# Kernel optimization log

Hardware: AMD Instinct MI355X
Metric: run time of the kernel (lower is better)

Reference implementation:

```python
import jax, jax.numpy as jnp
import numpy as np

B, T, L = 64, 512, 48
START, PAD, END = 46, 45, 47


def setup_inputs() -> dict:
    key = jax.random.key(0)
    k1, k2, k3 = jax.random.split(key, 3)
    scores = jax.random.normal(k1, (B, T, L), dtype=jnp.float32)
    gold_target = jax.random.randint(k2, (B, T), 0, L, dtype=jnp.int64)
    trans = jax.random.normal(k3, (L, L), dtype=jnp.float32)
    # replicate the in-place constraint initialization from __init__ (order matters)
    trans = trans.at[:, START].set(-10000.0)
    trans = trans.at[END, :].set(-10000.0)
    trans = trans.at[PAD, :].set(-10000.0)
    trans = trans.at[PAD, END].set(0.0)
    trans = trans.at[PAD, PAD].set(0.0)
    trans = trans.at[START, :].set(0.0)
    mask = jnp.ones((B, T), dtype=jnp.int32)
    return {"scores": scores, "gold_target": gold_target, "mask": mask, "transitions": trans}


def reference(scores, gold_target, mask, transitions):
    Bn, Tn, Ln = scores.shape
    # crf_scores[t, b, from, to] = emission(b, t, from) + transitions[from, to]  (time-major)
    crf = scores.transpose(1, 0, 2)[:, :, :, None] + transitions[None, None]      # (T, B, L, L)
    start = jnp.broadcast_to(transitions[None, None], (1, Bn, Ln, Ln))
    crf = jnp.concatenate([start, crf], axis=0)                                   # (T+1, B, L, L)

    # gold energy: faithful to original torch.gather on flattened (L*L) with raw tag index
    gold = jnp.concatenate(
        [jnp.full((1, Bn), START, dtype=gold_target.dtype), gold_target.T], axis=0)  # (T+1, B)
    flat = crf.reshape(Tn + 1, Bn, Ln * Ln)
    tg = jnp.take_along_axis(flat, gold[:, :, None], axis=2)[:, :, 0]             # (T+1, B)
    maskp = jnp.concatenate([jnp.ones((1, Bn), mask.dtype), mask.T], axis=0)      # (T+1, B)
    tg_energy = jnp.sum(tg * maskp.astype(tg.dtype))

    # forward algorithm (stable log-sum-exp recurrence) via lax.scan
    init = crf[0, :, START, :]                                                    # (B, L)
    def step(fs, xs):
        trans_t, m_t = xs                                                         # (B,L,L), (B,)
        nxt = jax.nn.logsumexp(fs[:, :, None] + trans_t, axis=1)                  # (B, L)
        fs = jnp.where(m_t[:, None].astype(bool), nxt, fs)
        return fs, None
    fs, _ = jax.lax.scan(step, init, (crf[1:], maskp[1:]))
    forscore = fs[:, END].sum()

    return (forscore - tg_energy) / Bn
```

## Files before the change

kernel.cpp:

```cpp
#include <hip/hip_runtime.h>

#define Bn 64
#define Tn 512
#define Ln 48
#define START_L 46
#define PAD_L 45
#define END_L 47
#define QP 72
#define LSEG 8
#define NBUF 16
#define NCHUNK (Tn / (LSEG * NBUF))

typedef __bf16 bf16x8 __attribute__((ext_vector_type(8)));
typedef float f32x4 __attribute__((ext_vector_type(4)));
#define MFMA __builtin_amdgcn_mfma_f32_16x16x32_bf16

__device__ __forceinline__ unsigned short f2bf(float x) {
    unsigned u = __float_as_uint(x);
    u += 0x7fffu + ((u >> 16) & 1u);
    return (unsigned short)(u >> 16);
}
__device__ __forceinline__ unsigned pkT(float a, float b) {
    return __builtin_amdgcn_perm(__float_as_uint(b), __float_as_uint(a), 0x07060302u);
}
__device__ __forceinline__ float bcast0(float x) {
    return __int_as_float(__builtin_amdgcn_readfirstlane(__float_as_int(x)));
}
__device__ __forceinline__ float4 exp4(float4 v) {
    float4 r; r.x = __expf(v.x); r.y = __expf(v.y); r.z = __expf(v.z); r.w = __expf(v.w);
    return r;
}


__device__ __forceinline__ void readTB(const unsigned short* buf, int c, int q, bf16x8 F[3][2]) {
    #pragma unroll
    for (int x = 0; x < 3; ++x) {
        F[x][0] = *(const bf16x8*)&buf[(x * 16 + c) * QP + q * 8];
        F[x][1] = *(const bf16x8*)&buf[(x * 16 + c) * QP + 32 + q * 8];
    }
}

__device__ __forceinline__ void storeTB(unsigned short* buf, int c, int q,
                                        const f32x4 (&acc)[3][3],
                                        float4 w0, float4 w1, float4 w2) {
    #pragma unroll
    for (int nt = 0; nt < 3; ++nt) {
        unsigned u0 = pkT(acc[0][nt][0] * w0.x, acc[0][nt][1] * w0.y);
        unsigned u1 = pkT(acc[0][nt][2] * w0.z, acc[0][nt][3] * w0.w);
        unsigned u2 = pkT(acc[1][nt][0] * w1.x, acc[1][nt][1] * w1.y);
        unsigned u3 = pkT(acc[1][nt][2] * w1.z, acc[1][nt][3] * w1.w);
        unsigned u4 = pkT(acc[2][nt][0] * w2.x, acc[2][nt][1] * w2.y);
        unsigned u5 = pkT(acc[2][nt][2] * w2.z, acc[2][nt][3] * w2.w);
        unsigned short* wp = &buf[(nt * 16 + c) * QP + q * 16];
        uint4 s4; s4.x = u0; s4.y = u1; s4.z = u2; s4.w = u3;
        *(uint4*)wp = s4;
        uint2 s2; s2.x = u4; s2.y = u5;
        *(uint2*)(wp + 8) = s2;
    }
}

__device__ __forceinline__ float treeProd(const unsigned short* bufA, const unsigned short* bufB,
                                          unsigned short* dst, int c, int q) {
    bf16x8 FA[3][2], FB[3][2];
    readTB(bufA, c, q, FA);
    readTB(bufB, c, q, FB);
    f32x4 acc[3][3];
    const f32x4 z = {0.f, 0.f, 0.f, 0.f};
    #pragma unroll
    for (int mt = 0; mt < 3; ++mt)
        #pragma unroll
        for (int nt = 0; nt < 3; ++nt) {
            acc[mt][nt] = MFMA(FA[mt][0], FB[nt][0], z, 0, 0, 0);
            acc[mt][nt] = MFMA(FA[mt][1], FB[nt][1], acc[mt][nt], 0, 0, 0);
        }
    float r = bcast0(acc[0][0][0]);
    float rr = __builtin_amdgcn_rcpf(r);
    float4 w; w.x = rr; w.y = rr; w.z = rr; w.w = rr;
    storeTB(dst, c, q, acc, w, w, w);
    return __logf(r);
}

__global__ __launch_bounds__(512, 2) void scan_k(
        const float* __restrict__ scores,
        const float* __restrict__ trans,
        unsigned short* __restrict__ ws2M,
        float* __restrict__ ws2S,
        float* __restrict__ out) {
    const int b   = blockIdx.x & (Bn - 1);
    const int cid = blockIdx.x >> 6;
    const int tid = threadIdx.x;
    const int w   = tid >> 6;
    const int lane = tid & 63;
    const int c = lane & 15;
    const int q = lane >> 4;

    __shared__ __align__(16) unsigned short TBs[NBUF][48 * QP];
    __shared__ float scl[32];

    for (int i = tid; i < NBUF * 48 * QP / 4; i += 512)
        ((unsigned long long*)TBs)[i] = 0ull;
    __syncthreads();

    const int dirOdd = w & 1;
    const int s1 = cid * NBUF + w;
    const int s2 = s1 + 8;
    const int t0a = s1 * LSEG, tea = t0a + LSEG - 1;
    const int t0b = s2 * LSEG, teb = t0b + LSEG - 1;
    const float* sb = scores + (size_t)b * Tn * Ln;

    bf16x8 A[3][2];
    #pragma unroll
    for (int mt = 0; mt < 3; ++mt)
        #pragma unroll
        for (int kt = 0; kt < 2; ++kt) {
            union { unsigned u[4]; bf16x8 v; } fu;
            #pragma unroll
            for (int j2 = 0; j2 < 4; ++j2) {
                int kk0 = kt * 32 + q * 8 + 2 * j2;
                int rem = kk0 & 15;
                if (rem < 12) {
                    int row0 = (rem >> 2) * 16 + (kk0 >> 4) * 4 + (kk0 & 3);
                    float tv0 = dirOdd ? trans[(mt * 16 + c) * Ln + row0]
                                       : trans[row0 * Ln + mt * 16 + c];
                    float tv1 = dirOdd ? trans[(mt * 16 + c) * Ln + row0 + 1]
                                       : trans[(row0 + 1) * Ln + mt * 16 + c];
                    fu.u[j2] = pkT(__expf(tv0), __expf(tv1));
                } else fu.u[j2] = 0u;
            }
            A[mt][kt] = fu.v;
        }

    unsigned short* TB0 = TBs[w];
    unsigned short* TB1 = TBs[w + 8];

    if (lane < Ln) {
        int m16 = lane >> 4, q4 = (lane >> 2) & 3, r = lane & 3;
        int kk = q4 * 16 + m16 * 4 + r;
        TB0[lane * QP + kk] = dirOdd ? (unsigned short)0x3F80
                                     : f2bf(__expf(sb[(size_t)t0a * Ln + lane]));
        TB1[lane * QP + kk] = dirOdd ? (unsigned short)0x3F80
                                     : f2bf(__expf(sb[(size_t)t0b * Ln + lane]));
    }

    auto clampA = [&](int t) { return t < t0a ? t0a : (t > tea ? tea : t); };
    auto clampB = [&](int t) { return t < t0b ? t0b : (t > teb ? teb : t); };

    float4 wA0, wA1, wA2, wB0, wB1, wB2;
    {
        const float* rp = sb + (size_t)(dirOdd ? tea : (t0a + 1)) * Ln;
        wA0 = exp4(*(const float4*)(rp + q * 4));
        wA1 = exp4(*(const float4*)(rp + 16 + q * 4));
        wA2 = exp4(*(const float4*)(rp + 32 + q * 4));
        const float* rp2 = sb + (size_t)(dirOdd ? teb : (t0b + 1)) * Ln;
        wB0 = exp4(*(const float4*)(rp2 + q * 4));
        wB1 = exp4(*(const float4*)(rp2 + 16 + q * 4));
        wB2 = exp4(*(const float4*)(rp2 + 32 + q * 4));
    }

    f32x4 acc0[3][3], acc1[3][3];
    float Cs0 = 0.f, Cs1 = 0.f;
    for (int tau = 0; tau < LSEG; ++tau) {
        bf16x8 Bf0[3][2], Bf1[3][2];
        readTB(TB0, c, q, Bf0);
        readTB(TB1, c, q, Bf1);

        int tnA = clampA(dirOdd ? (tea - (tau + 1)) : (t0a + 2 + tau));
        int tnB = clampB(dirOdd ? (teb - (tau + 1)) : (t0b + 2 + tau));
        const float* rpA = sb + (size_t)tnA * Ln;
        const float* rpB = sb + (size_t)tnB * Ln;
        float4 nA0 = *(const float4*)(rpA + q * 4);
        float4 nA1 = *(const float4*)(rpA + 16 + q * 4);
        float4 nA2 = *(const float4*)(rpA + 32 + q * 4);
        float4 nB0 = *(const float4*)(rpB + q * 4);
        float4 nB1 = *(const float4*)(rpB + 16 + q * 4);
        float4 nB2 = *(const float4*)(rpB + 32 + q * 4);

        const f32x4 z = {0.f, 0.f, 0.f, 0.f};
        #pragma unroll
        for (int mt = 0; mt < 3; ++mt)
            #pragma unroll
            for (int nt = 0; nt < 3; ++nt) {
                acc0[mt][nt] = MFMA(A[mt][0], Bf0[nt][0], z, 0, 0, 0);
                acc0[mt][nt] = MFMA(A[mt][1], Bf0[nt][1], acc0[mt][nt], 0, 0, 0);
            }
        #pragma unroll
        for (int mt = 0; mt < 3; ++mt)
            #pragma unroll
            for (int nt = 0; nt < 3; ++nt) {
                acc1[mt][nt] = MFMA(A[mt][0], Bf1[nt][0], z, 0, 0, 0);
                acc1[mt][nt] = MFMA(A[mt][1], Bf1[nt][1], acc1[mt][nt], 0, 0, 0);
            }

        const bool lastEven = (!dirOdd && tau == LSEG - 1);
        const bool doRenorm = (tau & 3) == 0;

        {
            float4 w0 = wA0, w1 = wA1, w2 = wA2;
            if (lastEven) { w0.x = w0.y = w0.z = w0.w = 1.f; w1 = w0; w2 = w0; }
            if (doRenorm) {
                float r = bcast0(acc0[0][0][0]);
                float rr = __builtin_amdgcn_rcpf(r);
                Cs0 += __logf(r);
                w0.x *= rr; w0.y *= rr; w0.z *= rr; w0.w *= rr;
                w1.x *= rr; w1.y *= rr; w1.z *= rr; w1.w *= rr;
                w2.x *= rr; w2.y *= rr; w2.z *= rr; w2.w *= rr;
            }
            storeTB(TB0, c, q, acc0, w0, w1, w2);
        }
        {
            float4 w0 = wB0, w1 = wB1, w2 = wB2;
            if (lastEven) { w0.x = w0.y = w0.z = w0.w = 1.f; w1 = w0; w2 = w0; }
            if (doRenorm) {
                float r = bcast0(acc1[0][0][0]);
                float rr = __builtin_amdgcn_rcpf(r);
                Cs1 += __logf(r);
                w0.x *= rr; w0.y *= rr; w0.z *= rr; w0.w *= rr;
                w1.x *= rr; w1.y *= rr; w1.z *= rr; w1.w *= rr;
                w2.x *= rr; w2.y *= rr; w2.z *= rr; w2.w *= rr;
            }
            storeTB(TB1, c, q, acc1, w0, w1, w2);
        }

        wA0 = exp4(nA0); wA1 = exp4(nA1); wA2 = exp4(nA2);
        wB0 = exp4(nB0); wB1 = exp4(nB1); wB2 = exp4(nB2);
    }
    if (lane == 0) { scl[w] = Cs0; scl[w + 8] = Cs1; }
    __syncthreads();

    {
        int i = w;
        const unsigned short* bufA = TBs[2 * i + ((i & 1) ? 0 : 1)];
        const unsigned short* bufB = TBs[2 * i + ((i & 1) ? 1 : 0)];
        float lg = treeProd(bufA, bufB, TBs[2 * i], c, q);
        if (lane == 0) scl[16 + i] = lg;
    }
    __syncthreads();
    if (w < 4) {
        int j = w;
        const unsigned short* bufA = TBs[4 * j + ((j & 1) ? 0 : 2)];
        const unsigned short* bufB = TBs[4 * j + ((j & 1) ? 2 : 0)];
        float lg = treeProd(bufA, bufB, TBs[4 * j], c, q);
        if (lane == 0) scl[24 + j] = lg;
    }
    __syncthreads();
    if (w < 2) {
        int p = w;
        const unsigned short* bufA = TBs[8 * p + ((p & 1) ? 0 : 4)];
        const unsigned short* bufB = TBs[8 * p + ((p & 1) ? 4 : 0)];
        float lg = treeProd(bufA, bufB, TBs[8 * p], c, q);
        if (lane == 0) scl[28 + p] = lg;
    }
    __syncthreads();
    if (w == 0) {
        bf16x8 FA[3][2], FB[3][2];
        readTB(TBs[8], c, q, FA);
        readTB(TBs[0], c, q, FB);
        f32x4 pac[3][3];
        const f32x4 z = {0.f, 0.f, 0.f, 0.f};
        #pragma unroll
        for (int mt = 0; mt < 3; ++mt)
            #pragma unroll
            for (int nt = 0; nt < 3; ++nt) {
                pac[mt][nt] = MFMA(FA[mt][0], FB[nt][0], z, 0, 0, 0);
                pac[mt][nt] = MFMA(FA[mt][1], FB[nt][1], pac[mt][nt], 0, 0, 0);
            }
        float r = bcast0(pac[0][0][0]);
        float rr = __builtin_amdgcn_rcpf(r);
        float Ct = __logf(r);
        #pragma unroll
        for (int i2 = 0; i2 < 30; ++i2) Ct += scl[i2];
        unsigned short* mp = ws2M + (size_t)blockIdx.x * (Ln * Ln);
        #pragma unroll
        for (int mt = 0; mt < 3; ++mt)
            #pragma unroll
            for (int nt = 0; nt < 3; ++nt)
                #pragma unroll
                for (int r2 = 0; r2 < 4; ++r2)
                    mp[(mt * 16 + q * 4 + r2) * Ln + nt * 16 + c] = f2bf(pac[mt][nt][r2] * rr);
        if (lane == 0) ws2S[blockIdx.x] = Ct;
    }
    if (blockIdx.x == 0 && tid == 0) out[0] = 0.f;
}

__global__ __launch_bounds__(64) void fin_k(
        const float* __restrict__ scores,
        const int* __restrict__ gold,
        const int* __restrict__ mask,
        const float* __restrict__ trans,
        const unsigned short* __restrict__ ws2M,
        const float* __restrict__ ws2S,
        float* __restrict__ out) {
    const int b = blockIdx.x;
    const int lane = threadIdx.x;
    const int j = (lane < Ln) ? lane : (Ln - 1);

    __shared__ float vB[64];

    float v = (lane < Ln) ? __expf(trans[START_L * Ln + lane]) : 0.0f;
    float Ctot = 0.0f;

    uint4 rows[NCHUNK][6];
    #pragma unroll
    for (int s2 = 0; s2 < NCHUNK; ++s2) {
        const unsigned short* p = ws2M + (size_t)(s2 * Bn + b) * (Ln * Ln) + (size_t)j * Ln;
        #pragma unroll
        for (int k = 0; k < 6; ++k) rows[s2][k] = *(const uint4*)(p + k * 8);
    }

    #pragma unroll
    for (int s2 = 0; s2 < NCHUNK; ++s2) {
        float Cs = ws2S[s2 * Bn + b];
        if (lane < Ln) vB[lane] = v;

        float a0 = 0.f, a1 = 0.f, a2 = 0.f, a3 = 0.f;
        #pragma unroll
        for (int k2 = 0; k2 < 12; ++k2) {
            float4 vb = *(const float4*)&vB[k2 * 4];
            uint4 ch = rows[s2][k2 >> 1];
            unsigned d0 = (k2 & 1) ? ch.z : ch.x;
            unsigned d1 = (k2 & 1) ? ch.w : ch.y;
            float f0 = __uint_as_float(d0 << 16);
            float f1 = __uint_as_float(d0 & 0xffff0000u);
            float f2 = __uint_as_float(d1 << 16);
            float f3 = __uint_as_float(d1 & 0xffff0000u);
            a0 = fmaf(f0, vb.x, a0);
            a1 = fmaf(f1, vb.y, a1);
            a2 = fmaf(f2, vb.z, a2);
            a3 = fmaf(f3, vb.w, a3);
        }
        float accv = (a0 + a1) + (a2 + a3);

        float r = bcast0(accv);
        v = accv * __builtin_amdgcn_rcpf(r);
        Ctot += __logf(r) + Cs;
    }

    if (lane == END_L) {
        atomicAdd(out, (__logf(v) + Ctot) * (1.0f / Bn));
    }

    float tgv = 0.0f;
    #pragma unroll
    for (int k = 0; k < Tn / 64; ++k) {
        int t = lane + k * 64;
        int idx = b * Tn + t;
        if (mask[idx]) tgv += scores[(size_t)idx * Ln] + trans[gold[idx]];
    }
    #pragma unroll
    for (int off = 32; off > 0; off >>= 1) tgv += __shfl_down(tgv, off);
    if (lane == 0) {
        float vv = -tgv * (1.0f / Bn);
        if (b == 0) vv -= trans[START_L];
        atomicAdd(out, vv);
    }
}

extern "C" void kernel_launch(void* const* d_in, const int* in_sizes, int n_in,
                              void* d_out, int out_size, void* d_ws, size_t ws_size,
                              hipStream_t stream) {
    const float* scores = (const float*)d_in[0];
    const int*   gold   = (const int*)d_in[1];
    const int*   mask   = (const int*)d_in[2];
    const float* trans  = (const float*)d_in[3];
    float* out = (float*)d_out;

    unsigned short* ws2M = (unsigned short*)d_ws;
    float* ws2S = (float*)((char*)d_ws + (size_t)Bn * NCHUNK * Ln * Ln * 2);

    scan_k<<<Bn * NCHUNK, 512, 0, stream>>>(scores, trans, ws2M, ws2S, out);
    fin_k<<<Bn, 64, 0, stream>>>(scores, gold, mask, trans, ws2M, ws2S, out);
}
```

Measured before the change: 90.09 us.

## Drop emission prefetch, renormalize once per segment, widen finalize kernel to four waves

The scan kernel no longer prefetches the next step's emission row a step ahead. It loads and exponentiates the current row inside the loop, which shortens live ranges and may lower register pressure at the cost of exposing load latency. Renormalization is cut from every fourth step to only the first step of each segment, removing log and reciprocal work but leaving less headroom against bf16/fp32 overflow over the segment. The finalize kernel now launches 256 threads so the gold-energy gather is spread over four waves with a shared-memory reduction, while wave 0 alone does the chunk matrix-vector chain.

```diff
diff --git a/kernel.cpp b/kernel.cpp
--- a/kernel.cpp
+++ b/kernel.cpp
@@ -142,39 +142,26 @@
                                      : f2bf(__expf(sb[(size_t)t0b * Ln + lane]));
     }
 
-    auto clampA = [&](int t) { return t < t0a ? t0a : (t > tea ? tea : t); };
-    auto clampB = [&](int t) { return t < t0b ? t0b : (t > teb ? teb : t); };
-
-    float4 wA0, wA1, wA2, wB0, wB1, wB2;
-    {
-        const float* rp = sb + (size_t)(dirOdd ? tea : (t0a + 1)) * Ln;
-        wA0 = exp4(*(const float4*)(rp + q * 4));
-        wA1 = exp4(*(const float4*)(rp + 16 + q * 4));
-        wA2 = exp4(*(const float4*)(rp + 32 + q * 4));
-        const float* rp2 = sb + (size_t)(dirOdd ? teb : (t0b + 1)) * Ln;
-        wB0 = exp4(*(const float4*)(rp2 + q * 4));
-        wB1 = exp4(*(const float4*)(rp2 + 16 + q * 4));
-        wB2 = exp4(*(const float4*)(rp2 + 32 + q * 4));
-    }
-
     f32x4 acc0[3][3], acc1[3][3];
     float Cs0 = 0.f, Cs1 = 0.f;
     for (int tau = 0; tau < LSEG; ++tau) {
+        int tA = dirOdd ? (tea - tau) : (t0a + 1 + tau);
+        if (tA > tea) tA = tea;
+        int tB = dirOdd ? (teb - tau) : (t0b + 1 + tau);
+        if (tB > teb) tB = teb;
+        const float* rpA = sb + (size_t)tA * Ln;
+        const float* rpB = sb + (size_t)tB * Ln;
+        float4 rA0 = *(const float4*)(rpA + q * 4);
+        float4 rA1 = *(const float4*)(rpA + 16 + q * 4);
+        float4 rA2 = *(const float4*)(rpA + 32 + q * 4);
+        float4 rB0 = *(const float4*)(rpB + q * 4);
+        float4 rB1 = *(const float4*)(rpB + 16 + q * 4);
+        float4 rB2 = *(const float4*)(rpB + 32 + q * 4);
+
         bf16x8 Bf0[3][2], Bf1[3][2];
         readTB(TB0, c, q, Bf0);
         readTB(TB1, c, q, Bf1);
 
-        int tnA = clampA(dirOdd ? (tea - (tau + 1)) : (t0a + 2 + tau));
-        int tnB = clampB(dirOdd ? (teb - (tau + 1)) : (t0b + 2 + tau));
-        const float* rpA = sb + (size_t)tnA * Ln;
-        const float* rpB = sb + (size_t)tnB * Ln;
-        float4 nA0 = *(const float4*)(rpA + q * 4);
-        float4 nA1 = *(const float4*)(rpA + 16 + q * 4);
-        float4 nA2 = *(const float4*)(rpA + 32 + q * 4);
-        float4 nB0 = *(const float4*)(rpB + q * 4);
-        float4 nB1 = *(const float4*)(rpB + 16 + q * 4);
-        float4 nB2 = *(const float4*)(rpB + 32 + q * 4);
-
         const f32x4 z = {0.f, 0.f, 0.f, 0.f};
         #pragma unroll
         for (int mt = 0; mt < 3; ++mt)
@@ -192,11 +179,15 @@
             }
 
         const bool lastEven = (!dirOdd && tau == LSEG - 1);
-        const bool doRenorm = (tau & 3) == 0;
+        const bool doRenorm = (tau == 0);
 
         {
-            float4 w0 = wA0, w1 = wA1, w2 = wA2;
-            if (lastEven) { w0.x = w0.y = w0.z = w0.w = 1.f; w1 = w0; w2 = w0; }
+            float4 w0, w1, w2;
+            if (lastEven) {
+                w0.x = w0.y = w0.z = w0.w = 1.f; w1 = w0; w2 = w0;
+            } else {
+                w0 = exp4(rA0); w1 = exp4(rA1); w2 = exp4(rA2);
+            }
             if (doRenorm) {
                 float r = bcast0(acc0[0][0][0]);
                 float rr = __builtin_amdgcn_rcpf(r);
@@ -208,8 +199,12 @@
             storeTB(TB0, c, q, acc0, w0, w1, w2);
         }
         {
-            float4 w0 = wB0, w1 = wB1, w2 = wB2;
-            if (lastEven) { w0.x = w0.y = w0.z = w0.w = 1.f; w1 = w0; w2 = w0; }
+            float4 w0, w1, w2;
+            if (lastEven) {
+                w0.x = w0.y = w0.z = w0.w = 1.f; w1 = w0; w2 = w0;
+            } else {
+                w0 = exp4(rB0); w1 = exp4(rB1); w2 = exp4(rB2);
+            }
             if (doRenorm) {
                 float r = bcast0(acc1[0][0][0]);
                 float rr = __builtin_amdgcn_rcpf(r);
@@ -220,9 +215,6 @@
             }
             storeTB(TB1, c, q, acc1, w0, w1, w2);
         }
-
-        wA0 = exp4(nA0); wA1 = exp4(nA1); wA2 = exp4(nA2);
-        wB0 = exp4(nB0); wB1 = exp4(nB1); wB2 = exp4(nB2);
     }
     if (lane == 0) { scl[w] = Cs0; scl[w + 8] = Cs1; }
     __syncthreads();
@@ -282,7 +274,7 @@
     if (blockIdx.x == 0 && tid == 0) out[0] = 0.f;
 }
 
-__global__ __launch_bounds__(64) void fin_k(
+__global__ __launch_bounds__(256) void fin_k(
         const float* __restrict__ scores,
         const int* __restrict__ gold,
         const int* __restrict__ mask,
@@ -291,67 +283,74 @@
         const float* __restrict__ ws2S,
         float* __restrict__ out) {
     const int b = blockIdx.x;
-    const int lane = threadIdx.x;
-    const int j = (lane < Ln) ? lane : (Ln - 1);
+    const int tid = threadIdx.x;
+    const int wv = tid >> 6;
+    const int lane = tid & 63;
 
     __shared__ float vB[64];
-
-    float v = (lane < Ln) ? __expf(trans[START_L * Ln + lane]) : 0.0f;
-    float Ctot = 0.0f;
-
-    uint4 rows[NCHUNK][6];
-    #pragma unroll
-    for (int s2 = 0; s2 < NCHUNK; ++s2) {
-        const unsigned short* p = ws2M + (size_t)(s2 * Bn + b) * (Ln * Ln) + (size_t)j * Ln;
-        #pragma unroll
-        for (int k = 0; k < 6; ++k) rows[s2][k] = *(const uint4*)(p + k * 8);
-    }
-
-    #pragma unroll
-    for (int s2 = 0; s2 < NCHUNK; ++s2) {
-        float Cs = ws2S[s2 * Bn + b];
-        if (lane < Ln) vB[lane] = v;
-
-        float a0 = 0.f, a1 = 0.f, a2 = 0.f, a3 = 0.f;
-        #pragma unroll
-        for (int k2 = 0; k2 < 12; ++k2) {
-            float4 vb = *(const float4*)&vB[k2 * 4];
-            uint4 ch = rows[s2][k2 >> 1];
-            unsigned d0 = (k2 & 1) ? ch.z : ch.x;
-            unsigned d1 = (k2 & 1) ? ch.w : ch.y;
-            float f0 = __uint_as_float(d0 << 16);
-            float f1 = __uint_as_float(d0 & 0xffff0000u);
-            float f2 = __uint_as_float(d1 << 16);
-            float f3 = __uint_as_float(d1 & 0xffff0000u);
-            a0 = fmaf(f0, vb.x, a0);
-            a1 = fmaf(f1, vb.y, a1);
-            a2 = fmaf(f2, vb.z, a2);
-            a3 = fmaf(f3, vb.w, a3);
-        }
-        float accv = (a0 + a1) + (a2 + a3);
-
-        float r = bcast0(accv);
-        v = accv * __builtin_amdgcn_rcpf(r);
-        Ctot += __logf(r) + Cs;
-    }
-
-    if (lane == END_L) {
-        atomicAdd(out, (__logf(v) + Ctot) * (1.0f / Bn));
-    }
+    __shared__ float gred[4];
 
     float tgv = 0.0f;
     #pragma unroll
-    for (int k = 0; k < Tn / 64; ++k) {
-        int t = lane + k * 64;
-        int idx = b * Tn + t;
+    for (int k = 0; k < 2; ++k) {
+        int idx = b * Tn + tid + k * 256;
         if (mask[idx]) tgv += scores[(size_t)idx * Ln] + trans[gold[idx]];
     }
     #pragma unroll
     for (int off = 32; off > 0; off >>= 1) tgv += __shfl_down(tgv, off);
-    if (lane == 0) {
-        float vv = -tgv * (1.0f / Bn);
+    if (lane == 0) gred[wv] = tgv;
+    __syncthreads();
+    if (tid == 0) {
+        float s = gred[0] + gred[1] + gred[2] + gred[3];
+        float vv = -s * (1.0f / Bn);
         if (b == 0) vv -= trans[START_L];
         atomicAdd(out, vv);
+    }
+
+    if (wv == 0) {
+        const int j = (lane < Ln) ? lane : (Ln - 1);
+        float v = (lane < Ln) ? __expf(trans[START_L * Ln + lane]) : 0.0f;
+        float Ctot = 0.0f;
+
+        uint4 rows[NCHUNK][6];
+        #pragma unroll
+        for (int s2 = 0; s2 < NCHUNK; ++s2) {
+            const unsigned short* p = ws2M + (size_t)(s2 * Bn + b) * (Ln * Ln) + (size_t)j * Ln;
+            #pragma unroll
+            for (int k = 0; k < 6; ++k) rows[s2][k] = *(const uint4*)(p + k * 8);
+        }
+
+        #pragma unroll
+        for (int s2 = 0; s2 < NCHUNK; ++s2) {
+            float Cs = ws2S[s2 * Bn + b];
+            if (lane < Ln) vB[lane] = v;
+
+            float a0 = 0.f, a1 = 0.f, a2 = 0.f, a3 = 0.f;
+            #pragma unroll
+            for (int k2 = 0; k2 < 12; ++k2) {
+                float4 vb = *(const float4*)&vB[k2 * 4];
+                uint4 ch = rows[s2][k2 >> 1];
+                unsigned d0 = (k2 & 1) ? ch.z : ch.x;
+                unsigned d1 = (k2 & 1) ? ch.w : ch.y;
+                float f0 = __uint_as_float(d0 << 16);
+                float f1 = __uint_as_float(d0 & 0xffff0000u);
+                float f2 = __uint_as_float(d1 << 16);
+                float f3 = __uint_as_float(d1 & 0xffff0000u);
+                a0 = fmaf(f0, vb.x, a0);
+                a1 = fmaf(f1, vb.y, a1);
+                a2 = fmaf(f2, vb.z, a2);
+                a3 = fmaf(f3, vb.w, a3);
+            }
+            float accv = (a0 + a1) + (a2 + a3);
+
+            float r = bcast0(accv);
+            v = accv * __builtin_amdgcn_rcpf(r);
+            Ctot += __logf(r) + Cs;
+        }
+
+        if (lane == END_L) {
+            atomicAdd(out, (__logf(v) + Ctot) * (1.0f / Bn));
+        }
     }
 }
 
@@ -368,5 +367,5 @@
     float* ws2S = (float*)((char*)d_ws + (size_t)Bn * NCHUNK * Ln * Ln * 2);
 
     scan_k<<<Bn * NCHUNK, 512, 0, stream>>>(scores, trans, ws2M, ws2S, out);
-    fin_k<<<Bn, 64, 0, stream>>>(scores, gold, mask, trans, ws2M, ws2S, out);
-}
+    fin_k<<<Bn, 256, 0, stream>>>(scores, gold, mask, trans, ws2M, ws2S, out);
+}
```

Result: faster. 87.54 us (-2.8%).
